# Optimization experiments

Hardware: AMD Instinct MI355X
Metric: run time of the kernel (lower is better)

Reference implementation:

```python
import jax, jax.numpy as jnp
import numpy as np

B, H, W = 8, 64, 64
D = 256          # in_dim == key_dim == value_dim
HEADS = 8
DK = D // HEADS  # per-head channels (key == value)
EPS = 1e-5


def _ln(x, g, b):
    m = jnp.mean(x, axis=-1, keepdims=True)
    v = jnp.var(x, axis=-1, keepdims=True)
    return (x - m) * jax.lax.rsqrt(v + EPS) * g + b


def setup_inputs() -> dict:
    key = jax.random.key(0)
    ks = jax.random.split(key, 8)
    return {
        "x1": jax.random.normal(ks[0], (B, H, W, 2 * D), jnp.float32),
        "x2": jax.random.normal(ks[1], (B, H, W, D), jnp.float32),
        "linear_w": jax.random.normal(ks[2], (2 * D, D), jnp.float32) * 0.02,
        "linear_b": jax.random.normal(ks[3], (D,), jnp.float32) * 0.02,
        "ln1_g": jnp.ones((D,), jnp.float32) + jax.random.normal(ks[4], (D,), jnp.float32) * 0.02,
        "ln1_b": jax.random.normal(ks[5], (D,), jnp.float32) * 0.02,
        "reproj_w": jax.random.normal(ks[6], (2 * D, D), jnp.float32) * 0.02,  # 1x1 conv kernel [out,in]
        "reproj_b": jax.random.normal(ks[7], (2 * D,), jnp.float32) * 0.02,
        "ln_attn_g": jnp.ones((2 * D,), jnp.float32),
        "ln_attn_b": jnp.zeros((2 * D,), jnp.float32),
    }


def _cross_attention(n1, n2, reproj_w, reproj_b, ln_g, ln_b):
    # n1 (values source), n2 (keys/queries source): [B,H,W,D]
    N = H * W
    v = n1.reshape(B, N, D).transpose(0, 2, 1).reshape(B, HEADS, DK, N)
    kq = n2.reshape(B, N, D).transpose(0, 2, 1).reshape(B, HEADS, DK, N)
    k = jax.nn.softmax(kq, axis=-1)  # softmax over tokens (dim=2 in torch slice)
    q = jax.nn.softmax(kq, axis=2)   # softmax over per-head channels (dim=1 in torch slice)
    # attended[b,h,d,n] = sum_m sum_e q[b,h,d,m] k[b,h,e,m] v[b,h,e,n]
    ctx = jnp.einsum('bhdm,bhem->bhde', q, k)          # [B,h,dk,dk]
    att = jnp.einsum('bhde,bhen->bhdn', ctx, v)        # [B,h,dk,N]
    agg = att.reshape(B, D, H, W)                      # concat heads along channels
    rep = jnp.einsum('od,bdhw->bohw', reproj_w, agg) + reproj_b[None, :, None, None]
    rep = rep.transpose(0, 2, 3, 1)                    # [B,H,W,2D]
    return _ln(rep, ln_g, ln_b)


def reference(x1, x2, linear_w, linear_b, ln1_g, ln1_b, reproj_w, reproj_b, ln_attn_g, ln_attn_b):
    n1 = _ln(x1 @ linear_w + linear_b, ln1_g, ln1_b)   # [B,H,W,D]
    n2 = _ln(x2, ln1_g, ln1_b)                          # [B,H,W,D]
    attn = _cross_attention(n1, n2, reproj_w, reproj_b, ln_attn_g, ln_attn_b)
    return x1 + attn
```

## Files before the change

kernel.cpp:

```cpp
#include <hip/hip_runtime.h>
#include <stdint.h>

typedef __bf16 bf16x8 __attribute__((ext_vector_type(8)));
typedef float f32x4 __attribute__((ext_vector_type(4)));

#define EPS 1e-5f

#define WAITVM(N) asm volatile("s_waitcnt vmcnt(" #N ")" ::: "memory")
#define WAITLGKM0 asm volatile("s_waitcnt lgkmcnt(0)" ::: "memory")

__device__ __forceinline__ void gl16(const void* g, void* l) {
    __builtin_amdgcn_global_load_lds(
        (const __attribute__((address_space(1))) unsigned int*)g,
        (__attribute__((address_space(3))) unsigned int*)l, 16, 0, 0);
}

__device__ __forceinline__ float b2f(unsigned short u) {
    union { unsigned int i; float f; } c; c.i = ((unsigned int)u) << 16; return c.f;
}
__device__ __forceinline__ unsigned short f2b(float f) {
    union { float f; unsigned int i; } c; c.f = f;
    unsigned int i = c.i;
    return (unsigned short)((i + 0x7FFFu + ((i >> 16) & 1u)) >> 16);
}

__global__ void k_zero(float* __restrict__ p, int n) {
    int i = blockIdx.x * 256 + threadIdx.x;
    if (i < n) p[i] = 0.0f;
}

__global__ void k_params(const float* __restrict__ lw, const float* __restrict__ rw,
                         const float* __restrict__ lb, const float* __restrict__ g1,
                         const float* __restrict__ b1, const float* __restrict__ rb,
                         const float* __restrict__ ga, const float* __restrict__ ba,
                         unsigned short* __restrict__ wt1,
                         unsigned short* __restrict__ rwb,
                         unsigned short* __restrict__ vec) {
    int gid = blockIdx.x * 256 + threadIdx.x;
    if (gid < 131072) {
        int k = gid >> 8, n = gid & 255;
        wt1[((size_t)(k >> 3) * 256 + n) * 8 + (k & 7)] = f2b(lw[gid]);
    } else if (gid < 262144) {
        int j = gid - 131072;
        rwb[j] = f2b(rw[j]);
    } else if (gid < 264448) {
        int j = gid - 262144;
        if (j < 256)       vec[j] = f2b(lb[j]);
        else if (j < 512)  vec[j] = f2b(g1[j - 256]);
        else if (j < 768)  vec[j] = f2b(b1[j - 512]);
        else if (j < 1280) vec[j] = f2b(rb[j - 768]);
        else if (j < 1792) vec[j] = f2b(ga[j - 1280]);
        else               vec[j] = f2b(ba[j - 1792]);
    }
}

__global__ __launch_bounds__(256) void k_stats(const float* __restrict__ x2,
                                               float2* __restrict__ stats) {
    int t = threadIdx.x, lane = t & 63, w = t >> 6;
    size_t row = (size_t)blockIdx.x * 4 + w;
    float4 f = *(const float4*)(x2 + row * 256 + lane * 4);
    float s = f.x + f.y + f.z + f.w;
    float q = f.x * f.x + f.y * f.y + f.z * f.z + f.w * f.w;
#pragma unroll
    for (int msk = 1; msk < 64; msk <<= 1) {
        s += __shfl_xor(s, msk, 64);
        q += __shfl_xor(q, msk, 64);
    }
    float mn = s * (1.0f / 256.0f);
    float rstd = rsqrtf(q * (1.0f / 256.0f) - mn * mn + EPS);
    if (lane == 0) stats[row] = make_float2(mn, rstd);
}

__global__ __launch_bounds__(256) void k_ctx(const float* __restrict__ x2,
                                             const float2* __restrict__ stats,
                                             const unsigned short* __restrict__ vec,
                                             float* __restrict__ ctxraw) {
    __shared__ float E[64 * 36];
    __shared__ float Q[64 * 36];
    __shared__ float gs[32], bs[32];
    int bh = blockIdx.x >> 3;
    int b = bh >> 3, h = bh & 7;
    int ch = blockIdx.x & 7;
    int t = threadIdx.x;
    if (t < 32) { gs[t] = b2f(vec[256 + h * 32 + t]); bs[t] = b2f(vec[512 + h * 32 + t]); }
    __syncthreads();
    int d = t >> 3, e0 = (t & 7) * 4;
    float a0 = 0.f, a1 = 0.f, a2 = 0.f, a3 = 0.f;
    const float* base = x2 + ((size_t)b * 4096 + ch * 512) * 256 + h * 32;
    int srow = b * 4096 + ch * 512;
    const int m = t >> 2, c0 = (t & 3) * 8;
    for (int s0 = 0; s0 < 512; s0 += 64) {
        float2 st = stats[srow + s0 + m];
        const float4* p = (const float4*)(base + (size_t)(s0 + m) * 256 + c0);
        float4 f0 = p[0], f1 = p[1];
        float ev[8];
        ev[0] = __expf((f0.x - st.x) * st.y * gs[c0 + 0] + bs[c0 + 0]);
        ev[1] = __expf((f0.y - st.x) * st.y * gs[c0 + 1] + bs[c0 + 1]);
        ev[2] = __expf((f0.z - st.x) * st.y * gs[c0 + 2] + bs[c0 + 2]);
        ev[3] = __expf((f0.w - st.x) * st.y * gs[c0 + 3] + bs[c0 + 3]);
        ev[4] = __expf((f1.x - st.x) * st.y * gs[c0 + 4] + bs[c0 + 4]);
        ev[5] = __expf((f1.y - st.x) * st.y * gs[c0 + 5] + bs[c0 + 5]);
        ev[6] = __expf((f1.z - st.x) * st.y * gs[c0 + 6] + bs[c0 + 6]);
        ev[7] = __expf((f1.w - st.x) * st.y * gs[c0 + 7] + bs[c0 + 7]);
        float ps = ev[0] + ev[1] + ev[2] + ev[3] + ev[4] + ev[5] + ev[6] + ev[7];
        ps += __shfl_xor(ps, 1, 64);
        ps += __shfl_xor(ps, 2, 64);
        float qi = 1.0f / ps;
        *(float4*)(E + m * 36 + c0)     = make_float4(ev[0], ev[1], ev[2], ev[3]);
        *(float4*)(E + m * 36 + c0 + 4) = make_float4(ev[4], ev[5], ev[6], ev[7]);
        *(float4*)(Q + m * 36 + c0)     = make_float4(ev[0]*qi, ev[1]*qi, ev[2]*qi, ev[3]*qi);
        *(float4*)(Q + m * 36 + c0 + 4) = make_float4(ev[4]*qi, ev[5]*qi, ev[6]*qi, ev[7]*qi);
        __syncthreads();
#pragma unroll 4
        for (int mm = 0; mm < 64; mm++) {
            float qd = Q[mm * 36 + d];
            float4 e4 = *(const float4*)(E + mm * 36 + e0);
            a0 += qd * e4.x; a1 += qd * e4.y; a2 += qd * e4.z; a3 += qd * e4.w;
        }
        __syncthreads();
    }
    float* dst = ctxraw + ((size_t)bh << 10) + (d << 5) + e0;
    atomicAdd(dst + 0, a0);
    atomicAdd(dst + 1, a1);
    atomicAdd(dst + 2, a2);
    atomicAdd(dst + 3, a3);
}

__global__ __launch_bounds__(256) void k_w2(const float* __restrict__ ctxraw,
                                            const unsigned short* __restrict__ rwb,
                                            unsigned short* __restrict__ w2t) {
    __shared__ float ctx_s[1024];
    __shared__ float cinv[32];
    int blk = blockIdx.x;
    int b = blk >> 6, h = (blk >> 3) & 7, os = blk & 7;
    int bh = b * 8 + h;
    int t = threadIdx.x;
#pragma unroll
    for (int i = 0; i < 4; i++) ctx_s[t + 256 * i] = ctxraw[((size_t)bh << 10) + t + 256 * i];
    __syncthreads();
    if (t < 32) {
        float s = 0.f;
#pragma unroll
        for (int d = 0; d < 32; d++) s += ctx_s[d * 32 + t];
        cinv[t] = 1.0f / s;
    }
    __syncthreads();
    int o = os * 64 + (t >> 2);
    int e0 = (t & 3) * 8;
    float wv[32];
    const uint4* wp = (const uint4*)(rwb + (size_t)o * 256 + h * 32);
#pragma unroll
    for (int qd = 0; qd < 4; qd++) {
        uint4 u = wp[qd];
        unsigned int uu[4] = {u.x, u.y, u.z, u.w};
#pragma unroll
        for (int j = 0; j < 4; j++) {
            wv[qd * 8 + j * 2]     = b2f((unsigned short)(uu[j] & 0xFFFFu));
            wv[qd * 8 + j * 2 + 1] = b2f((unsigned short)(uu[j] >> 16));
        }
    }
    float s[8];
#pragma unroll
    for (int j = 0; j < 8; j++) s[j] = 0.f;
#pragma unroll 8
    for (int d = 0; d < 32; d++) {
        float w = wv[d];
#pragma unroll
        for (int j = 0; j < 8; j++) s[j] += ctx_s[d * 32 + e0 + j] * w;
    }
    ushort4 o4a, o4b;
    o4a.x = f2b(s[0] * cinv[e0 + 0]); o4a.y = f2b(s[1] * cinv[e0 + 1]);
    o4a.z = f2b(s[2] * cinv[e0 + 2]); o4a.w = f2b(s[3] * cinv[e0 + 3]);
    o4b.x = f2b(s[4] * cinv[e0 + 4]); o4b.y = f2b(s[5] * cinv[e0 + 5]);
    o4b.z = f2b(s[6] * cinv[e0 + 6]); o4b.w = f2b(s[7] * cinv[e0 + 7]);
    int kb = h * 4 + (e0 >> 3);
    unsigned short* dst = w2t + (size_t)b * 131072 + ((size_t)kb * 512 + o) * 8;
    *(ushort4*)dst = o4a;
    *(ushort4*)(dst + 4) = o4b;
}

__global__ __launch_bounds__(512, 1) void k_fused(
    const float* __restrict__ x1, const unsigned short* __restrict__ wt1,
    const unsigned short* __restrict__ w2t, const unsigned short* __restrict__ vec,
    float* __restrict__ out) {
    extern __shared__ __align__(16) char pool[];
    unsigned short* n1s = (unsigned short*)pool;
    char* Breg = pool + 67584;

    const int t = threadIdx.x;
    const int lane = t & 63, w = t >> 6;
    const int l15 = lane & 15, quad = lane >> 4;
    const int rb = blockIdx.x;
    const int row0 = rb << 7;
    const char* wt1c = (const char*)wt1;
    const char* wbase = (const char*)w2t + (size_t)(rb >> 5) * 262144;

    const float* xrow = x1 + (size_t)(row0 + (w << 4) + l15) * 512 + quad * 8;

    f32x4 acc[16];
#pragma unroll
    for (int i = 0; i < 16; i++) acc[i] = (f32x4){0.f, 0.f, 0.f, 0.f};

#pragma unroll
    for (int i = 0; i < 2; i++)
        gl16(wt1c + ((w * 2 + i) << 10) + lane * 16,
             Breg + ((w * 2 + i) << 10) + lane * 16);
    float4 fa[2][2];
    fa[0][0] = *(const float4*)xrow;
    fa[0][1] = *(const float4*)(xrow + 4);

#pragma unroll
    for (int s = 0; s < 16; ++s) {
        const int cur = s & 1;
        if (s < 15) {
            const float* xn = xrow + (s + 1) * 32;
            fa[cur ^ 1][0] = *(const float4*)xn;
            fa[cur ^ 1][1] = *(const float4*)(xn + 4);
#pragma unroll
            for (int i = 0; i < 2; i++)
                gl16(wt1c + (size_t)(s + 1) * 16384 + ((w * 2 + i) << 10) + lane * 16,
                     Breg + (cur ^ 1) * 16384 + ((w * 2 + i) << 10) + lane * 16);
        }
        bf16x8 af;
        af[0] = (__bf16)fa[cur][0].x; af[1] = (__bf16)fa[cur][0].y;
        af[2] = (__bf16)fa[cur][0].z; af[3] = (__bf16)fa[cur][0].w;
        af[4] = (__bf16)fa[cur][1].x; af[5] = (__bf16)fa[cur][1].y;
        af[6] = (__bf16)fa[cur][1].z; af[7] = (__bf16)fa[cur][1].w;
        if (s < 15) { WAITVM(4); } else { WAITVM(0); }
        __builtin_amdgcn_s_barrier();
        const char* Bc = Breg + cur * 16384 + quad * 4096 + l15 * 16;
#pragma unroll
        for (int cb = 0; cb < 16; cb++) {
            bf16x8 bf = *(const bf16x8*)(Bc + cb * 256);
            acc[cb] = __builtin_amdgcn_mfma_f32_16x16x32_bf16(af, bf, acc[cb], 0, 0, 0);
        }
        WAITLGKM0;
        __builtin_amdgcn_s_barrier();
    }

    float bc_[16], gg_[16], bb_[16];
#pragma unroll
    for (int cb = 0; cb < 16; cb++) {
        int col = (cb << 4) + l15;
        bc_[cb] = b2f(vec[col]);
        gg_[cb] = b2f(vec[256 + col]);
        bb_[cb] = b2f(vec[512 + col]);
    }
#pragma unroll
    for (int i = 0; i < 4; i++)
        gl16(wbase + ((w * 4 + i) << 10) + lane * 16,
             Breg + 32768 + ((w * 4 + i) << 10) + lane * 16);

#pragma unroll
    for (int cb = 0; cb < 16; cb++) {
#pragma unroll
        for (int r = 0; r < 4; r++) acc[cb][r] += bc_[cb];
    }
    float mean_[4], rstd_[4];
#pragma unroll
    for (int r = 0; r < 4; r++) {
        float s = 0.f, q = 0.f;
#pragma unroll
        for (int cb = 0; cb < 16; cb++) { float v = acc[cb][r]; s += v; q += v * v; }
#pragma unroll
        for (int msk = 1; msk < 16; msk <<= 1) {
            s += __shfl_xor(s, msk, 64);
            q += __shfl_xor(q, msk, 64);
        }
        float mn = s * (1.0f / 256.0f);
        mean_[r] = mn;
        rstd_[r] = rsqrtf(q * (1.0f / 256.0f) - mn * mn + EPS);
    }
#pragma unroll
    for (int cb = 0; cb < 16; cb++) {
        int col = (cb << 4) + l15;
#pragma unroll
        for (int r = 0; r < 4; r++) {
            int rr = (w << 4) + (quad << 2) + r;
            n1s[rr * 264 + col] =
                f2b((acc[cb][r] - mean_[r]) * rstd_[r] * gg_[cb] + bb_[cb]);
        }
    }
    WAITLGKM0;
    __builtin_amdgcn_s_barrier();

    f32x4 acc2[32];
#pragma unroll
    for (int i = 0; i < 32; i++) acc2[i] = (f32x4){0.f, 0.f, 0.f, 0.f};
    const unsigned short* an1 = n1s + ((w << 4) + l15) * 264 + quad * 8;

#pragma unroll
    for (int s = 0; s < 8; ++s) {
        const char* bufc = Breg + ((s & 1) ? 0 : 32768);
        if (s < 7) {
            char* bufn = Breg + (((s + 1) & 1) ? 0 : 32768);
#pragma unroll
            for (int i = 0; i < 4; i++)
                gl16(wbase + (size_t)(s + 1) * 32768 + ((w * 4 + i) << 10) + lane * 16,
                     bufn + ((w * 4 + i) << 10) + lane * 16);
        }
        bf16x8 a2 = *(const bf16x8*)(an1 + s * 32);
        if (s < 7) { WAITVM(4); } else { WAITVM(0); }
        __builtin_amdgcn_s_barrier();
        const char* Bc = bufc + quad * 8192 + l15 * 16;
#pragma unroll
        for (int cb = 0; cb < 32; cb++) {
            bf16x8 bf = *(const bf16x8*)(Bc + cb * 256);
            acc2[cb] = __builtin_amdgcn_mfma_f32_16x16x32_bf16(a2, bf, acc2[cb], 0, 0, 0);
        }
        WAITLGKM0;
        __builtin_amdgcn_s_barrier();
    }

#pragma unroll
    for (int cb = 0; cb < 32; cb++) {
        float bc = b2f(vec[768 + (cb << 4) + l15]);
#pragma unroll
        for (int r = 0; r < 4; r++) acc2[cb][r] += bc;
    }
    float mean2[4], rstd2[4];
#pragma unroll
    for (int r = 0; r < 4; r++) {
        float s = 0.f, q = 0.f;
#pragma unroll
        for (int cb = 0; cb < 32; cb++) { float v = acc2[cb][r]; s += v; q += v * v; }
#pragma unroll
        for (int msk = 1; msk < 16; msk <<= 1) {
            s += __shfl_xor(s, msk, 64);
            q += __shfl_xor(q, msk, 64);
        }
        float mn = s * (1.0f / 512.0f);
        mean2[r] = mn;
        rstd2[r] = rsqrtf(q * (1.0f / 512.0f) - mn * mn + EPS);
    }
    float* rep = (float*)pool;
    const int hfw = w >> 2;
#pragma unroll
    for (int hv = 0; hv < 2; ++hv) {
        if (hv) __builtin_amdgcn_s_barrier();
        if (hfw == hv) {
#pragma unroll
            for (int cb = 0; cb < 32; cb++) {
                int col = (cb << 4) + l15;
                float gg = b2f(vec[1280 + col]), bbv = b2f(vec[1792 + col]);
                int rl = ((w & 3) << 4) + (quad << 2);
#pragma unroll
                for (int r = 0; r < 4; r++)
                    rep[(rl + r) * 516 + col] =
                        (acc2[cb][r] - mean2[r]) * rstd2[r] * gg + bbv;
            }
        }
        WAITLGKM0;
        __builtin_amdgcn_s_barrier();
        int rr = t >> 4, c0 = (t & 15) << 2;
#pragma unroll
        for (int j = 0; j < 8; j++) {
            int col = c0 + (j << 6);
            float4 v0 = *(const float4*)(rep + rr * 516 + col);
            float4 v1 = *(const float4*)(rep + (rr + 32) * 516 + col);
            size_t g0 = (size_t)(row0 + (hv << 6) + rr) * 512 + col;
            size_t g1 = g0 + (size_t)32 * 512;
            float4 xa = *(const float4*)(x1 + g0);
            float4 xb = *(const float4*)(x1 + g1);
            v0.x += xa.x; v0.y += xa.y; v0.z += xa.z; v0.w += xa.w;
            v1.x += xb.x; v1.y += xb.y; v1.z += xb.z; v1.w += xb.w;
            *(float4*)(out + g0) = v0;
            *(float4*)(out + g1) = v1;
        }
        WAITLGKM0;
        __builtin_amdgcn_s_barrier();
    }
}

extern "C" void kernel_launch(void* const* d_in, const int* in_sizes, int n_in,
                              void* d_out, int out_size, void* d_ws, size_t ws_size,
                              hipStream_t stream) {
    const float* x1 = (const float*)d_in[0];
    const float* x2 = (const float*)d_in[1];
    const float* lw = (const float*)d_in[2];
    const float* lb = (const float*)d_in[3];
    const float* g1 = (const float*)d_in[4];
    const float* b1 = (const float*)d_in[5];
    const float* rw = (const float*)d_in[6];
    const float* rb = (const float*)d_in[7];
    const float* ga = (const float*)d_in[8];
    const float* ba = (const float*)d_in[9];
    float* out = (float*)d_out;

    char* ws = (char*)d_ws;
    float*          ctxr  = (float*)(ws);
    float2*         stats = (float2*)(ws + 262144);
    unsigned short* wt1   = (unsigned short*)(ws + 524288);
    unsigned short* rwb   = (unsigned short*)(ws + 786432);
    unsigned short* vec   = (unsigned short*)(ws + 1048576);
    unsigned short* w2t   = (unsigned short*)(ws + 1064960);

    static bool attr_set = false;
    if (!attr_set) {
        hipFuncSetAttribute((const void*)k_fused,
                            hipFuncAttributeMaxDynamicSharedMemorySize, 133120);
        attr_set = true;
    }

    k_zero<<<dim3(256), dim3(256), 0, stream>>>(ctxr, 65536);
    k_params<<<dim3(1033), dim3(256), 0, stream>>>(lw, rw, lb, g1, b1, rb, ga, ba,
                                                   wt1, rwb, vec);
    k_stats<<<dim3(8192), dim3(256), 0, stream>>>(x2, stats);
    k_ctx<<<dim3(512), dim3(256), 0, stream>>>(x2, stats, vec, ctxr);
    k_w2<<<dim3(512), dim3(256), 0, stream>>>(ctxr, rwb, w2t);
    k_fused<<<dim3(256), dim3(512), 133120, stream>>>(x1, wt1, w2t, vec, out);
}
```

Before: 228.8 us.

## Halve fused block tile and load reprojection weights directly from global

The fused kernel now uses 256-thread blocks covering 64 rows each, launching 512 blocks with half the LDS, so two blocks can fit per CU. The second GEMM no longer stages per-batch weights through LDS with double buffering. Each wave reads B fragments straight from global/L2 and computes a 32x256 tile, which reuses every B load across two row sub-tiles. The 512-wide layernorm is now split across two waves and merged through a small shared reduction buffer. This trades LDS staging and barriers for more global/L2 traffic and higher register pressure from 32 accumulators.

```diff
diff --git a/kernel.cpp b/kernel.cpp
--- a/kernel.cpp
+++ b/kernel.cpp
@@ -179,21 +179,23 @@
     *(ushort4*)(dst + 4) = o4b;
 }
 
-__global__ __launch_bounds__(512, 1) void k_fused(
+__global__ __launch_bounds__(256, 2) void k_fused(
     const float* __restrict__ x1, const unsigned short* __restrict__ wt1,
     const unsigned short* __restrict__ w2t, const unsigned short* __restrict__ vec,
     float* __restrict__ out) {
     extern __shared__ __align__(16) char pool[];
     unsigned short* n1s = (unsigned short*)pool;
-    char* Breg = pool + 67584;
+    char* Breg = pool + 33792;
+    __shared__ float2 red[64][2];
 
     const int t = threadIdx.x;
     const int lane = t & 63, w = t >> 6;
     const int l15 = lane & 15, quad = lane >> 4;
+    const int wr = w >> 1, wc = w & 1;
     const int rb = blockIdx.x;
-    const int row0 = rb << 7;
+    const int row0 = rb << 6;
     const char* wt1c = (const char*)wt1;
-    const char* wbase = (const char*)w2t + (size_t)(rb >> 5) * 262144;
+    const char* wbase = (const char*)w2t + (size_t)(rb >> 6) * 262144;
 
     const float* xrow = x1 + (size_t)(row0 + (w << 4) + l15) * 512 + quad * 8;
 
@@ -202,9 +204,8 @@
     for (int i = 0; i < 16; i++) acc[i] = (f32x4){0.f, 0.f, 0.f, 0.f};
 
 #pragma unroll
-    for (int i = 0; i < 2; i++)
-        gl16(wt1c + ((w * 2 + i) << 10) + lane * 16,
-             Breg + ((w * 2 + i) << 10) + lane * 16);
+    for (int i = 0; i < 4; i++)
+        gl16(wt1c + i * 4096 + t * 16, Breg + i * 4096 + t * 16);
     float4 fa[2][2];
     fa[0][0] = *(const float4*)xrow;
     fa[0][1] = *(const float4*)(xrow + 4);
@@ -217,22 +218,22 @@
             fa[cur ^ 1][0] = *(const float4*)xn;
             fa[cur ^ 1][1] = *(const float4*)(xn + 4);
 #pragma unroll
-            for (int i = 0; i < 2; i++)
-                gl16(wt1c + (size_t)(s + 1) * 16384 + ((w * 2 + i) << 10) + lane * 16,
-                     Breg + (cur ^ 1) * 16384 + ((w * 2 + i) << 10) + lane * 16);
+            for (int i = 0; i < 4; i++)
+                gl16(wt1c + (size_t)(s + 1) * 16384 + i * 4096 + t * 16,
+                     Breg + (cur ^ 1) * 16384 + i * 4096 + t * 16);
         }
         bf16x8 af;
         af[0] = (__bf16)fa[cur][0].x; af[1] = (__bf16)fa[cur][0].y;
         af[2] = (__bf16)fa[cur][0].z; af[3] = (__bf16)fa[cur][0].w;
         af[4] = (__bf16)fa[cur][1].x; af[5] = (__bf16)fa[cur][1].y;
         af[6] = (__bf16)fa[cur][1].z; af[7] = (__bf16)fa[cur][1].w;
-        if (s < 15) { WAITVM(4); } else { WAITVM(0); }
+        if (s < 15) { WAITVM(6); } else { WAITVM(0); }
         __builtin_amdgcn_s_barrier();
         const char* Bc = Breg + cur * 16384 + quad * 4096 + l15 * 16;
 #pragma unroll
-        for (int cb = 0; cb < 16; cb++) {
-            bf16x8 bf = *(const bf16x8*)(Bc + cb * 256);
-            acc[cb] = __builtin_amdgcn_mfma_f32_16x16x32_bf16(af, bf, acc[cb], 0, 0, 0);
+        for (int nb = 0; nb < 16; nb++) {
+            bf16x8 bf = *(const bf16x8*)(Bc + nb * 256);
+            acc[nb] = __builtin_amdgcn_mfma_f32_16x16x32_bf16(af, bf, acc[nb], 0, 0, 0);
         }
         WAITLGKM0;
         __builtin_amdgcn_s_barrier();
@@ -240,28 +241,23 @@
 
     float bc_[16], gg_[16], bb_[16];
 #pragma unroll
-    for (int cb = 0; cb < 16; cb++) {
-        int col = (cb << 4) + l15;
-        bc_[cb] = b2f(vec[col]);
-        gg_[cb] = b2f(vec[256 + col]);
-        bb_[cb] = b2f(vec[512 + col]);
-    }
-#pragma unroll
-    for (int i = 0; i < 4; i++)
-        gl16(wbase + ((w * 4 + i) << 10) + lane * 16,
-             Breg + 32768 + ((w * 4 + i) << 10) + lane * 16);
-
-#pragma unroll
-    for (int cb = 0; cb < 16; cb++) {
-#pragma unroll
-        for (int r = 0; r < 4; r++) acc[cb][r] += bc_[cb];
+    for (int nb = 0; nb < 16; nb++) {
+        int col = (nb << 4) + l15;
+        bc_[nb] = b2f(vec[col]);
+        gg_[nb] = b2f(vec[256 + col]);
+        bb_[nb] = b2f(vec[512 + col]);
+    }
+#pragma unroll
+    for (int nb = 0; nb < 16; nb++) {
+#pragma unroll
+        for (int r = 0; r < 4; r++) acc[nb][r] += bc_[nb];
     }
     float mean_[4], rstd_[4];
 #pragma unroll
     for (int r = 0; r < 4; r++) {
         float s = 0.f, q = 0.f;
 #pragma unroll
-        for (int cb = 0; cb < 16; cb++) { float v = acc[cb][r]; s += v; q += v * v; }
+        for (int nb = 0; nb < 16; nb++) { float v = acc[nb][r]; s += v; q += v * v; }
 #pragma unroll
         for (int msk = 1; msk < 16; msk <<= 1) {
             s += __shfl_xor(s, msk, 64);
@@ -272,103 +268,111 @@
         rstd_[r] = rsqrtf(q * (1.0f / 256.0f) - mn * mn + EPS);
     }
 #pragma unroll
-    for (int cb = 0; cb < 16; cb++) {
-        int col = (cb << 4) + l15;
+    for (int nb = 0; nb < 16; nb++) {
+        int col = (nb << 4) + l15;
 #pragma unroll
         for (int r = 0; r < 4; r++) {
             int rr = (w << 4) + (quad << 2) + r;
             n1s[rr * 264 + col] =
-                f2b((acc[cb][r] - mean_[r]) * rstd_[r] * gg_[cb] + bb_[cb]);
-        }
-    }
-    WAITLGKM0;
-    __builtin_amdgcn_s_barrier();
-
-    f32x4 acc2[32];
-#pragma unroll
-    for (int i = 0; i < 32; i++) acc2[i] = (f32x4){0.f, 0.f, 0.f, 0.f};
-    const unsigned short* an1 = n1s + ((w << 4) + l15) * 264 + quad * 8;
-
-#pragma unroll
+                f2b((acc[nb][r] - mean_[r]) * rstd_[r] * gg_[nb] + bb_[nb]);
+        }
+    }
+    __syncthreads();
+
+    f32x4 acc2[2][16];
+#pragma unroll
+    for (int m = 0; m < 2; m++)
+#pragma unroll
+        for (int nb = 0; nb < 16; nb++) acc2[m][nb] = (f32x4){0.f, 0.f, 0.f, 0.f};
+    const unsigned short* an0 = n1s + ((wr << 5) + l15) * 264 + quad * 8;
+    const char* bq = wbase + quad * 8192 + ((wc << 8) + l15) * 16;
+
     for (int s = 0; s < 8; ++s) {
-        const char* bufc = Breg + ((s & 1) ? 0 : 32768);
-        if (s < 7) {
-            char* bufn = Breg + (((s + 1) & 1) ? 0 : 32768);
-#pragma unroll
-            for (int i = 0; i < 4; i++)
-                gl16(wbase + (size_t)(s + 1) * 32768 + ((w * 4 + i) << 10) + lane * 16,
-                     bufn + ((w * 4 + i) << 10) + lane * 16);
-        }
-        bf16x8 a2 = *(const bf16x8*)(an1 + s * 32);
-        if (s < 7) { WAITVM(4); } else { WAITVM(0); }
-        __builtin_amdgcn_s_barrier();
-        const char* Bc = bufc + quad * 8192 + l15 * 16;
-#pragma unroll
-        for (int cb = 0; cb < 32; cb++) {
-            bf16x8 bf = *(const bf16x8*)(Bc + cb * 256);
-            acc2[cb] = __builtin_amdgcn_mfma_f32_16x16x32_bf16(a2, bf, acc2[cb], 0, 0, 0);
-        }
-        WAITLGKM0;
-        __builtin_amdgcn_s_barrier();
-    }
-
-#pragma unroll
-    for (int cb = 0; cb < 32; cb++) {
-        float bc = b2f(vec[768 + (cb << 4) + l15]);
-#pragma unroll
-        for (int r = 0; r < 4; r++) acc2[cb][r] += bc;
-    }
-    float mean2[4], rstd2[4];
-#pragma unroll
-    for (int r = 0; r < 4; r++) {
-        float s = 0.f, q = 0.f;
-#pragma unroll
-        for (int cb = 0; cb < 32; cb++) { float v = acc2[cb][r]; s += v; q += v * v; }
-#pragma unroll
-        for (int msk = 1; msk < 16; msk <<= 1) {
-            s += __shfl_xor(s, msk, 64);
-            q += __shfl_xor(q, msk, 64);
-        }
-        float mn = s * (1.0f / 512.0f);
-        mean2[r] = mn;
-        rstd2[r] = rsqrtf(q * (1.0f / 512.0f) - mn * mn + EPS);
-    }
+        bf16x8 a0 = *(const bf16x8*)(an0 + s * 32);
+        bf16x8 a1 = *(const bf16x8*)(an0 + 16 * 264 + s * 32);
+        const char* bs8 = bq + (size_t)s * 32768;
+#pragma unroll
+        for (int nb = 0; nb < 16; nb++) {
+            bf16x8 bf = *(const bf16x8*)(bs8 + nb * 256);
+            acc2[0][nb] = __builtin_amdgcn_mfma_f32_16x16x32_bf16(a0, bf, acc2[0][nb], 0, 0, 0);
+            acc2[1][nb] = __builtin_amdgcn_mfma_f32_16x16x32_bf16(a1, bf, acc2[1][nb], 0, 0, 0);
+        }
+    }
+
+    float rb_[16], ga_[16], ba_[16];
+#pragma unroll
+    for (int nb = 0; nb < 16; nb++) {
+        int col = (wc << 8) + (nb << 4) + l15;
+        rb_[nb] = b2f(vec[768 + col]);
+        ga_[nb] = b2f(vec[1280 + col]);
+        ba_[nb] = b2f(vec[1792 + col]);
+    }
+#pragma unroll
+    for (int m = 0; m < 2; m++)
+#pragma unroll
+        for (int nb = 0; nb < 16; nb++)
+#pragma unroll
+            for (int r = 0; r < 4; r++) acc2[m][nb][r] += rb_[nb];
+
+#pragma unroll
+    for (int m = 0; m < 2; m++)
+#pragma unroll
+        for (int r = 0; r < 4; r++) {
+            float s = 0.f, q = 0.f;
+#pragma unroll
+            for (int nb = 0; nb < 16; nb++) { float v = acc2[m][nb][r]; s += v; q += v * v; }
+#pragma unroll
+            for (int msk = 1; msk < 16; msk <<= 1) {
+                s += __shfl_xor(s, msk, 64);
+                q += __shfl_xor(q, msk, 64);
+            }
+            if (l15 == 0)
+                red[(wr << 5) + (m << 4) + (quad << 2) + r][wc] = make_float2(s, q);
+        }
+    __syncthreads();
+    float mean2[2][4], rstd2[2][4];
+#pragma unroll
+    for (int m = 0; m < 2; m++)
+#pragma unroll
+        for (int r = 0; r < 4; r++) {
+            int rr = (wr << 5) + (m << 4) + (quad << 2) + r;
+            float2 cA = red[rr][0], cB = red[rr][1];
+            float s = cA.x + cB.x, q = cA.y + cB.y;
+            float mn = s * (1.0f / 512.0f);
+            mean2[m][r] = mn;
+            rstd2[m][r] = rsqrtf(q * (1.0f / 512.0f) - mn * mn + EPS);
+        }
     float* rep = (float*)pool;
-    const int hfw = w >> 2;
 #pragma unroll
     for (int hv = 0; hv < 2; ++hv) {
-        if (hv) __builtin_amdgcn_s_barrier();
-        if (hfw == hv) {
-#pragma unroll
-            for (int cb = 0; cb < 32; cb++) {
-                int col = (cb << 4) + l15;
-                float gg = b2f(vec[1280 + col]), bbv = b2f(vec[1792 + col]);
-                int rl = ((w & 3) << 4) + (quad << 2);
-#pragma unroll
-                for (int r = 0; r < 4; r++)
-                    rep[(rl + r) * 516 + col] =
-                        (acc2[cb][r] - mean2[r]) * rstd2[r] * gg + bbv;
+        if (hv) __syncthreads();
+        if (wc == hv) {
+#pragma unroll
+            for (int m = 0; m < 2; m++)
+#pragma unroll
+                for (int nb = 0; nb < 16; nb++) {
+                    int col = (nb << 4) + l15;
+                    int rl = (wr << 5) + (m << 4) + (quad << 2);
+#pragma unroll
+                    for (int r = 0; r < 4; r++)
+                        rep[(rl + r) * 260 + col] =
+                            (acc2[m][nb][r] - mean2[m][r]) * rstd2[m][r] * ga_[nb] + ba_[nb];
+                }
+        }
+        __syncthreads();
+#pragma unroll
+        for (int rg = 0; rg < 4; rg++) {
+            int row = (rg << 4) + (t >> 4);
+#pragma unroll
+            for (int j = 0; j < 4; j++) {
+                int col = ((t & 15) << 2) + (j << 6);
+                float4 v = *(const float4*)(rep + row * 260 + col);
+                size_t g = (size_t)(row0 + row) * 512 + (hv << 8) + col;
+                float4 xa = *(const float4*)(x1 + g);
+                v.x += xa.x; v.y += xa.y; v.z += xa.z; v.w += xa.w;
+                *(float4*)(out + g) = v;
             }
         }
-        WAITLGKM0;
-        __builtin_amdgcn_s_barrier();
-        int rr = t >> 4, c0 = (t & 15) << 2;
-#pragma unroll
-        for (int j = 0; j < 8; j++) {
-            int col = c0 + (j << 6);
-            float4 v0 = *(const float4*)(rep + rr * 516 + col);
-            float4 v1 = *(const float4*)(rep + (rr + 32) * 516 + col);
-            size_t g0 = (size_t)(row0 + (hv << 6) + rr) * 512 + col;
-            size_t g1 = g0 + (size_t)32 * 512;
-            float4 xa = *(const float4*)(x1 + g0);
-            float4 xb = *(const float4*)(x1 + g1);
-            v0.x += xa.x; v0.y += xa.y; v0.z += xa.z; v0.w += xa.w;
-            v1.x += xb.x; v1.y += xb.y; v1.z += xb.z; v1.w += xb.w;
-            *(float4*)(out + g0) = v0;
-            *(float4*)(out + g1) = v1;
-        }
-        WAITLGKM0;
-        __builtin_amdgcn_s_barrier();
     }
 }
 
@@ -398,7 +402,7 @@
     static bool attr_set = false;
     if (!attr_set) {
         hipFuncSetAttribute((const void*)k_fused,
-                            hipFuncAttributeMaxDynamicSharedMemorySize, 133120);
+                            hipFuncAttributeMaxDynamicSharedMemorySize, 66560);
         attr_set = true;
     }
 
@@ -408,5 +412,5 @@
     k_stats<<<dim3(8192), dim3(256), 0, stream>>>(x2, stats);
     k_ctx<<<dim3(512), dim3(256), 0, stream>>>(x2, stats, vec, ctxr);
     k_w2<<<dim3(512), dim3(256), 0, stream>>>(ctxr, rwb, w2t);
-    k_fused<<<dim3(256), dim3(512), 133120, stream>>>(x1, wt1, w2t, vec, out);
-}
+    k_fused<<<dim3(512), dim3(256), 66560, stream>>>(x1, wt1, w2t, vec, out);
+}
```

Result: slower. 244.1 us (+6.7%).

## Merge prep, stats, ctx and w2 kernels into one cooperative kernel with grid syncs

Applied to the files above, without the earlier changes.

Replaces five small preprocessing launches (zero, params conversion, LN stats, context accumulation, reprojection weight fold) with one cooperative kernel of 512 blocks separated by grid-wide syncs. The goal is to remove per-launch overhead and inter-kernel gaps. In exchange it adds two grid barriers, needs all 512 blocks co-resident (two per CU), and each block now does 16 rows of stats serially instead of spreading that work over many small blocks.

```diff
diff --git a/kernel.cpp b/kernel.cpp
--- a/kernel.cpp
+++ b/kernel.cpp
@@ -1,5 +1,8 @@
 #include <hip/hip_runtime.h>
+#include <hip/hip_cooperative_groups.h>
 #include <stdint.h>
+
+namespace cg = cooperative_groups;
 
 typedef __bf16 bf16x8 __attribute__((ext_vector_type(8)));
 typedef float f32x4 __attribute__((ext_vector_type(4)));
@@ -24,159 +27,160 @@
     return (unsigned short)((i + 0x7FFFu + ((i >> 16) & 1u)) >> 16);
 }
 
-__global__ void k_zero(float* __restrict__ p, int n) {
-    int i = blockIdx.x * 256 + threadIdx.x;
-    if (i < n) p[i] = 0.0f;
-}
-
-__global__ void k_params(const float* __restrict__ lw, const float* __restrict__ rw,
-                         const float* __restrict__ lb, const float* __restrict__ g1,
-                         const float* __restrict__ b1, const float* __restrict__ rb,
-                         const float* __restrict__ ga, const float* __restrict__ ba,
-                         unsigned short* __restrict__ wt1,
-                         unsigned short* __restrict__ rwb,
-                         unsigned short* __restrict__ vec) {
-    int gid = blockIdx.x * 256 + threadIdx.x;
-    if (gid < 131072) {
-        int k = gid >> 8, n = gid & 255;
-        wt1[((size_t)(k >> 3) * 256 + n) * 8 + (k & 7)] = f2b(lw[gid]);
-    } else if (gid < 262144) {
-        int j = gid - 131072;
-        rwb[j] = f2b(rw[j]);
-    } else if (gid < 264448) {
-        int j = gid - 262144;
-        if (j < 256)       vec[j] = f2b(lb[j]);
-        else if (j < 512)  vec[j] = f2b(g1[j - 256]);
-        else if (j < 768)  vec[j] = f2b(b1[j - 512]);
-        else if (j < 1280) vec[j] = f2b(rb[j - 768]);
-        else if (j < 1792) vec[j] = f2b(ga[j - 1280]);
-        else               vec[j] = f2b(ba[j - 1792]);
-    }
-}
-
-__global__ __launch_bounds__(256) void k_stats(const float* __restrict__ x2,
-                                               float2* __restrict__ stats) {
-    int t = threadIdx.x, lane = t & 63, w = t >> 6;
-    size_t row = (size_t)blockIdx.x * 4 + w;
-    float4 f = *(const float4*)(x2 + row * 256 + lane * 4);
-    float s = f.x + f.y + f.z + f.w;
-    float q = f.x * f.x + f.y * f.y + f.z * f.z + f.w * f.w;
-#pragma unroll
-    for (int msk = 1; msk < 64; msk <<= 1) {
-        s += __shfl_xor(s, msk, 64);
-        q += __shfl_xor(q, msk, 64);
-    }
-    float mn = s * (1.0f / 256.0f);
-    float rstd = rsqrtf(q * (1.0f / 256.0f) - mn * mn + EPS);
-    if (lane == 0) stats[row] = make_float2(mn, rstd);
-}
-
-__global__ __launch_bounds__(256) void k_ctx(const float* __restrict__ x2,
-                                             const float2* __restrict__ stats,
-                                             const unsigned short* __restrict__ vec,
-                                             float* __restrict__ ctxraw) {
+__global__ __launch_bounds__(256, 2) void k_attn(
+    const float* __restrict__ x2,
+    const float* __restrict__ lw, const float* __restrict__ rw,
+    const float* __restrict__ lb, const float* __restrict__ g1,
+    const float* __restrict__ b1, const float* __restrict__ rb,
+    const float* __restrict__ ga, const float* __restrict__ ba,
+    unsigned short* __restrict__ wt1, unsigned short* __restrict__ rwb,
+    unsigned short* __restrict__ vec, float2* __restrict__ stats,
+    float* __restrict__ ctxr, unsigned short* __restrict__ w2t) {
     __shared__ float E[64 * 36];
     __shared__ float Q[64 * 36];
     __shared__ float gs[32], bs[32];
-    int bh = blockIdx.x >> 3;
-    int b = bh >> 3, h = bh & 7;
-    int ch = blockIdx.x & 7;
-    int t = threadIdx.x;
-    if (t < 32) { gs[t] = b2f(vec[256 + h * 32 + t]); bs[t] = b2f(vec[512 + h * 32 + t]); }
-    __syncthreads();
-    int d = t >> 3, e0 = (t & 7) * 4;
-    float a0 = 0.f, a1 = 0.f, a2 = 0.f, a3 = 0.f;
-    const float* base = x2 + ((size_t)b * 4096 + ch * 512) * 256 + h * 32;
-    int srow = b * 4096 + ch * 512;
-    const int m = t >> 2, c0 = (t & 3) * 8;
-    for (int s0 = 0; s0 < 512; s0 += 64) {
-        float2 st = stats[srow + s0 + m];
-        const float4* p = (const float4*)(base + (size_t)(s0 + m) * 256 + c0);
-        float4 f0 = p[0], f1 = p[1];
-        float ev[8];
-        ev[0] = __expf((f0.x - st.x) * st.y * gs[c0 + 0] + bs[c0 + 0]);
-        ev[1] = __expf((f0.y - st.x) * st.y * gs[c0 + 1] + bs[c0 + 1]);
-        ev[2] = __expf((f0.z - st.x) * st.y * gs[c0 + 2] + bs[c0 + 2]);
-        ev[3] = __expf((f0.w - st.x) * st.y * gs[c0 + 3] + bs[c0 + 3]);
-        ev[4] = __expf((f1.x - st.x) * st.y * gs[c0 + 4] + bs[c0 + 4]);
-        ev[5] = __expf((f1.y - st.x) * st.y * gs[c0 + 5] + bs[c0 + 5]);
-        ev[6] = __expf((f1.z - st.x) * st.y * gs[c0 + 6] + bs[c0 + 6]);
-        ev[7] = __expf((f1.w - st.x) * st.y * gs[c0 + 7] + bs[c0 + 7]);
-        float ps = ev[0] + ev[1] + ev[2] + ev[3] + ev[4] + ev[5] + ev[6] + ev[7];
-        ps += __shfl_xor(ps, 1, 64);
-        ps += __shfl_xor(ps, 2, 64);
-        float qi = 1.0f / ps;
-        *(float4*)(E + m * 36 + c0)     = make_float4(ev[0], ev[1], ev[2], ev[3]);
-        *(float4*)(E + m * 36 + c0 + 4) = make_float4(ev[4], ev[5], ev[6], ev[7]);
-        *(float4*)(Q + m * 36 + c0)     = make_float4(ev[0]*qi, ev[1]*qi, ev[2]*qi, ev[3]*qi);
-        *(float4*)(Q + m * 36 + c0 + 4) = make_float4(ev[4]*qi, ev[5]*qi, ev[6]*qi, ev[7]*qi);
-        __syncthreads();
-#pragma unroll 4
-        for (int mm = 0; mm < 64; mm++) {
-            float qd = Q[mm * 36 + d];
-            float4 e4 = *(const float4*)(E + mm * 36 + e0);
-            a0 += qd * e4.x; a1 += qd * e4.y; a2 += qd * e4.z; a3 += qd * e4.w;
-        }
-        __syncthreads();
-    }
-    float* dst = ctxraw + ((size_t)bh << 10) + (d << 5) + e0;
-    atomicAdd(dst + 0, a0);
-    atomicAdd(dst + 1, a1);
-    atomicAdd(dst + 2, a2);
-    atomicAdd(dst + 3, a3);
-}
-
-__global__ __launch_bounds__(256) void k_w2(const float* __restrict__ ctxraw,
-                                            const unsigned short* __restrict__ rwb,
-                                            unsigned short* __restrict__ w2t) {
     __shared__ float ctx_s[1024];
     __shared__ float cinv[32];
-    int blk = blockIdx.x;
-    int b = blk >> 6, h = (blk >> 3) & 7, os = blk & 7;
-    int bh = b * 8 + h;
-    int t = threadIdx.x;
-#pragma unroll
-    for (int i = 0; i < 4; i++) ctx_s[t + 256 * i] = ctxraw[((size_t)bh << 10) + t + 256 * i];
-    __syncthreads();
-    if (t < 32) {
-        float s = 0.f;
-#pragma unroll
-        for (int d = 0; d < 32; d++) s += ctx_s[d * 32 + t];
-        cinv[t] = 1.0f / s;
-    }
-    __syncthreads();
-    int o = os * 64 + (t >> 2);
-    int e0 = (t & 3) * 8;
-    float wv[32];
-    const uint4* wp = (const uint4*)(rwb + (size_t)o * 256 + h * 32);
-#pragma unroll
-    for (int qd = 0; qd < 4; qd++) {
-        uint4 u = wp[qd];
-        unsigned int uu[4] = {u.x, u.y, u.z, u.w};
-#pragma unroll
-        for (int j = 0; j < 4; j++) {
-            wv[qd * 8 + j * 2]     = b2f((unsigned short)(uu[j] & 0xFFFFu));
-            wv[qd * 8 + j * 2 + 1] = b2f((unsigned short)(uu[j] >> 16));
-        }
-    }
-    float s[8];
-#pragma unroll
-    for (int j = 0; j < 8; j++) s[j] = 0.f;
+    cg::grid_group grid = cg::this_grid();
+    const int bid = blockIdx.x;
+    const int t = threadIdx.x;
+    const int lane = t & 63, w = t >> 6;
+
+#pragma unroll 4
+    for (int it = 0; it < 16; ++it) {
+        size_t row = (size_t)bid * 64 + it * 4 + w;
+        float4 f = *(const float4*)(x2 + row * 256 + lane * 4);
+        float s = f.x + f.y + f.z + f.w;
+        float q = f.x * f.x + f.y * f.y + f.z * f.z + f.w * f.w;
+#pragma unroll
+        for (int msk = 1; msk < 64; msk <<= 1) {
+            s += __shfl_xor(s, msk, 64);
+            q += __shfl_xor(q, msk, 64);
+        }
+        float mn = s * (1.0f / 256.0f);
+        float rstd = rsqrtf(q * (1.0f / 256.0f) - mn * mn + EPS);
+        if (lane == 0) stats[row] = make_float2(mn, rstd);
+    }
+
+    for (int gid = bid * 256 + t; gid < 329984; gid += 131072) {
+        if (gid < 131072) {
+            int k = gid >> 8, n = gid & 255;
+            wt1[((size_t)(k >> 3) * 256 + n) * 8 + (k & 7)] = f2b(lw[gid]);
+        } else if (gid < 262144) {
+            int j = gid - 131072;
+            rwb[j] = f2b(rw[j]);
+        } else if (gid < 264448) {
+            int j = gid - 262144;
+            if (j < 256)       vec[j] = f2b(lb[j]);
+            else if (j < 512)  vec[j] = f2b(g1[j - 256]);
+            else if (j < 768)  vec[j] = f2b(b1[j - 512]);
+            else if (j < 1280) vec[j] = f2b(rb[j - 768]);
+            else if (j < 1792) vec[j] = f2b(ga[j - 1280]);
+            else               vec[j] = f2b(ba[j - 1792]);
+        } else {
+            ctxr[gid - 264448] = 0.0f;
+        }
+    }
+    __threadfence();
+    grid.sync();
+
+    {
+        int bh = bid >> 3;
+        int b = bh >> 3, h = bh & 7;
+        int ch = bid & 7;
+        if (t < 32) { gs[t] = b2f(vec[256 + h * 32 + t]); bs[t] = b2f(vec[512 + h * 32 + t]); }
+        __syncthreads();
+        int d = t >> 3, e0 = (t & 7) * 4;
+        float a0 = 0.f, a1 = 0.f, a2 = 0.f, a3 = 0.f;
+        const float* base = x2 + ((size_t)b * 4096 + ch * 512) * 256 + h * 32;
+        int srow = b * 4096 + ch * 512;
+        const int m = t >> 2, c0 = (t & 3) * 8;
+        for (int s0 = 0; s0 < 512; s0 += 64) {
+            float2 st = stats[srow + s0 + m];
+            const float4* p = (const float4*)(base + (size_t)(s0 + m) * 256 + c0);
+            float4 f0 = p[0], f1 = p[1];
+            float ev[8];
+            ev[0] = __expf((f0.x - st.x) * st.y * gs[c0 + 0] + bs[c0 + 0]);
+            ev[1] = __expf((f0.y - st.x) * st.y * gs[c0 + 1] + bs[c0 + 1]);
+            ev[2] = __expf((f0.z - st.x) * st.y * gs[c0 + 2] + bs[c0 + 2]);
+            ev[3] = __expf((f0.w - st.x) * st.y * gs[c0 + 3] + bs[c0 + 3]);
+            ev[4] = __expf((f1.x - st.x) * st.y * gs[c0 + 4] + bs[c0 + 4]);
+            ev[5] = __expf((f1.y - st.x) * st.y * gs[c0 + 5] + bs[c0 + 5]);
+            ev[6] = __expf((f1.z - st.x) * st.y * gs[c0 + 6] + bs[c0 + 6]);
+            ev[7] = __expf((f1.w - st.x) * st.y * gs[c0 + 7] + bs[c0 + 7]);
+            float ps = ev[0] + ev[1] + ev[2] + ev[3] + ev[4] + ev[5] + ev[6] + ev[7];
+            ps += __shfl_xor(ps, 1, 64);
+            ps += __shfl_xor(ps, 2, 64);
+            float qi = 1.0f / ps;
+            *(float4*)(E + m * 36 + c0)     = make_float4(ev[0], ev[1], ev[2], ev[3]);
+            *(float4*)(E + m * 36 + c0 + 4) = make_float4(ev[4], ev[5], ev[6], ev[7]);
+            *(float4*)(Q + m * 36 + c0)     = make_float4(ev[0]*qi, ev[1]*qi, ev[2]*qi, ev[3]*qi);
+            *(float4*)(Q + m * 36 + c0 + 4) = make_float4(ev[4]*qi, ev[5]*qi, ev[6]*qi, ev[7]*qi);
+            __syncthreads();
+#pragma unroll 4
+            for (int mm = 0; mm < 64; mm++) {
+                float qd = Q[mm * 36 + d];
+                float4 e4 = *(const float4*)(E + mm * 36 + e0);
+                a0 += qd * e4.x; a1 += qd * e4.y; a2 += qd * e4.z; a3 += qd * e4.w;
+            }
+            __syncthreads();
+        }
+        float* dst = ctxr + ((size_t)bh << 10) + (d << 5) + e0;
+        atomicAdd(dst + 0, a0);
+        atomicAdd(dst + 1, a1);
+        atomicAdd(dst + 2, a2);
+        atomicAdd(dst + 3, a3);
+    }
+    __threadfence();
+    grid.sync();
+
+    {
+        int blk = bid;
+        int b = blk >> 6, h = (blk >> 3) & 7, os = blk & 7;
+        int bh = b * 8 + h;
+#pragma unroll
+        for (int i = 0; i < 4; i++) ctx_s[t + 256 * i] = ctxr[((size_t)bh << 10) + t + 256 * i];
+        __syncthreads();
+        if (t < 32) {
+            float s = 0.f;
+#pragma unroll
+            for (int d = 0; d < 32; d++) s += ctx_s[d * 32 + t];
+            cinv[t] = 1.0f / s;
+        }
+        __syncthreads();
+        int o = os * 64 + (t >> 2);
+        int e0 = (t & 3) * 8;
+        float wv[32];
+        const uint4* wp = (const uint4*)(rwb + (size_t)o * 256 + h * 32);
+#pragma unroll
+        for (int qd = 0; qd < 4; qd++) {
+            uint4 u = wp[qd];
+            unsigned int uu[4] = {u.x, u.y, u.z, u.w};
+#pragma unroll
+            for (int j = 0; j < 4; j++) {
+                wv[qd * 8 + j * 2]     = b2f((unsigned short)(uu[j] & 0xFFFFu));
+                wv[qd * 8 + j * 2 + 1] = b2f((unsigned short)(uu[j] >> 16));
+            }
+        }
+        float s[8];
+#pragma unroll
+        for (int j = 0; j < 8; j++) s[j] = 0.f;
 #pragma unroll 8
-    for (int d = 0; d < 32; d++) {
-        float w = wv[d];
-#pragma unroll
-        for (int j = 0; j < 8; j++) s[j] += ctx_s[d * 32 + e0 + j] * w;
-    }
-    ushort4 o4a, o4b;
-    o4a.x = f2b(s[0] * cinv[e0 + 0]); o4a.y = f2b(s[1] * cinv[e0 + 1]);
-    o4a.z = f2b(s[2] * cinv[e0 + 2]); o4a.w = f2b(s[3] * cinv[e0 + 3]);
-    o4b.x = f2b(s[4] * cinv[e0 + 4]); o4b.y = f2b(s[5] * cinv[e0 + 5]);
-    o4b.z = f2b(s[6] * cinv[e0 + 6]); o4b.w = f2b(s[7] * cinv[e0 + 7]);
-    int kb = h * 4 + (e0 >> 3);
-    unsigned short* dst = w2t + (size_t)b * 131072 + ((size_t)kb * 512 + o) * 8;
-    *(ushort4*)dst = o4a;
-    *(ushort4*)(dst + 4) = o4b;
+        for (int d = 0; d < 32; d++) {
+            float wd = wv[d];
+#pragma unroll
+            for (int j = 0; j < 8; j++) s[j] += ctx_s[d * 32 + e0 + j] * wd;
+        }
+        ushort4 o4a, o4b;
+        o4a.x = f2b(s[0] * cinv[e0 + 0]); o4a.y = f2b(s[1] * cinv[e0 + 1]);
+        o4a.z = f2b(s[2] * cinv[e0 + 2]); o4a.w = f2b(s[3] * cinv[e0 + 3]);
+        o4b.x = f2b(s[4] * cinv[e0 + 4]); o4b.y = f2b(s[5] * cinv[e0 + 5]);
+        o4b.z = f2b(s[6] * cinv[e0 + 6]); o4b.w = f2b(s[7] * cinv[e0 + 7]);
+        int kb = h * 4 + (e0 >> 3);
+        unsigned short* dst = w2t + (size_t)b * 131072 + ((size_t)kb * 512 + o) * 8;
+        *(ushort4*)dst = o4a;
+        *(ushort4*)(dst + 4) = o4b;
+    }
 }
 
 __global__ __launch_bounds__(512, 1) void k_fused(
@@ -402,11 +406,11 @@
         attr_set = true;
     }
 
-    k_zero<<<dim3(256), dim3(256), 0, stream>>>(ctxr, 65536);
-    k_params<<<dim3(1033), dim3(256), 0, stream>>>(lw, rw, lb, g1, b1, rb, ga, ba,
-                                                   wt1, rwb, vec);
-    k_stats<<<dim3(8192), dim3(256), 0, stream>>>(x2, stats);
-    k_ctx<<<dim3(512), dim3(256), 0, stream>>>(x2, stats, vec, ctxr);
-    k_w2<<<dim3(512), dim3(256), 0, stream>>>(ctxr, rwb, w2t);
+    void* kargs[] = {
+        (void*)&x2, (void*)&lw, (void*)&rw, (void*)&lb, (void*)&g1, (void*)&b1,
+        (void*)&rb, (void*)&ga, (void*)&ba, (void*)&wt1, (void*)&rwb, (void*)&vec,
+        (void*)&stats, (void*)&ctxr, (void*)&w2t
+    };
+    hipLaunchCooperativeKernel((void*)k_attn, dim3(512), dim3(256), kargs, 0, stream);
     k_fused<<<dim3(256), dim3(512), 133120, stream>>>(x1, wt1, w2t, vec, out);
 }
```

Measured after the change: 411.8 us. +80.0%, slower.
